# Kernel tuning notes

Measured on AMD Instinct MI355X. Metric: run time of the kernel, lower is better.

The kernel has to match this reference:

```python
import jax, jax.numpy as jnp
import numpy as np

BETA = 0.95
THRESH = 1.0
T = 25
MAXD = 11      # dilated_kernel_size: 250//25=10 -> bumped to odd 11
LP = 10        # left_pad = 250//25
B = 1024
SIGINIT = 5.0  # max_delay // 2, SIG is frozen at this value


@jax.custom_vjp
def atan_spike(u):
    # heaviside forward, atan surrogate gradient (snntorch surrogate.atan, alpha=2)
    return (u > 0).astype(u.dtype)

def _atan_fwd(u):
    return atan_spike(u), u

def _atan_bwd(u, g):
    return (g / (1.0 + (jnp.pi * u) ** 2),)

atan_spike.defvjp(_atan_fwd, _atan_bwd)


def dcls_kernel(W, P, SIG):
    # DCLS 'gauss': gaussian-interpolated dense kernel.
    # W: (O, I, kc), P/SIG: (1, O, I, kc) -> dense kernel (O, I, MAXD)
    idx = jnp.arange(MAXD, dtype=W.dtype)
    Pc = P[0] + MAXD // 2                      # center positions in dense kernel
    S = jnp.abs(SIG[0]) + 0.27                 # sigma floor (DCLS epsilon)
    X = jnp.exp(-0.5 * ((idx[:, None, None, None] - Pc) / S) ** 2)  # (K,O,I,kc)
    X = X / (X.sum(axis=0, keepdims=True) + 1e-7)
    return jnp.einsum('oic,joic->oij', W, X)


def dcls_conv(x, W, P, SIG, b):
    # x: (B, C_in, L) -> (B, C_out, L - MAXD + 1), VALID conv like padding=0
    k = dcls_kernel(W, P, SIG)
    y = jax.lax.conv_general_dilated(x, k, (1,), 'VALID',
                                     dimension_numbers=('NCH', 'OIH', 'NCH'))
    return y + b[None, :, None]


def batchnorm(x, gamma, beta, mean, var, eps=1e-5):
    # eval-mode BatchNorm1d over (B, C, L)
    inv = gamma / jnp.sqrt(var + eps)
    return (x - mean[None, :, None]) * inv[None, :, None] + beta[None, :, None]


def lif_scan(x):
    # snntorch Leaky, reset_mechanism='subtract'; x: (B, C, T) input currents
    xT = jnp.moveaxis(x, 2, 0)  # (T, B, C)

    def step(mem, xt):
        reset = jax.lax.stop_gradient(atan_spike(mem - THRESH))  # detached reset
        mem = BETA * mem + xt - reset * THRESH
        spk = atan_spike(mem - THRESH)
        return mem, (spk, mem)

    _, (spk, mem) = jax.lax.scan(step, jnp.zeros_like(xT[0]), xT)
    return spk, mem  # each (T, B, C)


def pad_left(x):
    return jnp.pad(x, ((0, 0), (0, 0), (LP, 0)))


def setup_inputs() -> dict:
    key = jax.random.key(0)
    ks = jax.random.split(key, 16)

    def w_init(k, o, i):
        return jax.random.normal(k, (o, i, 1), jnp.float32) / np.sqrt(i)

    inp = {
        'data': jax.random.normal(ks[0], (B, T, 140), jnp.float32),
        'W1': w_init(ks[1], 256, 140),
        'b1': jax.random.normal(ks[2], (256,), jnp.float32) * 0.01,
        'P1': jax.random.uniform(ks[3], (1, 256, 140, 1), jnp.float32, -SIGINIT, SIGINIT),
        'SIG1': jnp.full((1, 256, 140, 1), SIGINIT, jnp.float32),
        'bn1_gamma': jax.random.uniform(ks[4], (256,), jnp.float32, 0.5, 1.5),
        'bn1_beta': jax.random.normal(ks[5], (256,), jnp.float32) * 0.1,
        'bn1_mean': jax.random.normal(ks[6], (256,), jnp.float32) * 0.1,
        'bn1_var': jax.random.uniform(ks[7], (256,), jnp.float32, 0.5, 1.5),
        'W2': w_init(ks[8], 256, 256),
        'b2': jax.random.normal(ks[9], (256,), jnp.float32) * 0.01,
        'P2': jax.random.uniform(ks[10], (1, 256, 256, 1), jnp.float32, -SIGINIT, SIGINIT),
        'SIG2': jnp.full((1, 256, 256, 1), SIGINIT, jnp.float32),
        'bn2_gamma': jax.random.uniform(ks[11], (256,), jnp.float32, 0.5, 1.5),
        'bn2_beta': jax.random.normal(ks[12], (256,), jnp.float32) * 0.1,
        'bn2_mean': jax.random.normal(ks[13], (256,), jnp.float32) * 0.1,
        'bn2_var': jax.random.uniform(ks[14], (256,), jnp.float32, 0.5, 1.5),
        'W3': w_init(ks[15], 20, 256),
        'b3': jnp.zeros((20,), jnp.float32),
        'P3': jax.random.uniform(jax.random.fold_in(key, 99), (1, 20, 256, 1), jnp.float32, -SIGINIT, SIGINIT),
        'SIG3': jnp.full((1, 20, 256, 1), SIGINIT, jnp.float32),
    }
    return inp


def reference(data, W1, b1, P1, SIG1, bn1_gamma, bn1_beta, bn1_mean, bn1_var,
              W2, b2, P2, SIG2, bn2_gamma, bn2_beta, bn2_mean, bn2_var,
              W3, b3, P3, SIG3):
    # data: (B, T, 140); pad time dim on the left, then to (B, C, L)
    x = jnp.moveaxis(jnp.pad(data, ((0, 0), (LP, 0), (0, 0))), 1, 2)  # (B,140,T+LP)
    x = batchnorm(dcls_conv(x, W1, P1, SIG1, b1), bn1_gamma, bn1_beta, bn1_mean, bn1_var)
    spk1, _ = lif_scan(x)                  # (T, B, 256)
    in1 = jnp.moveaxis(spk1, 0, 2)         # (B, 256, T)  (dropout eval = identity)

    x = batchnorm(dcls_conv(pad_left(in1), W2, P2, SIG2, b2),
                  bn2_gamma, bn2_beta, bn2_mean, bn2_var)
    spk2, _ = lif_scan(x)
    in2 = jnp.moveaxis(spk2, 0, 2)         # (B, 256, T)

    x = dcls_conv(pad_left(in2), W3, P3, SIG3, b3)  # (B, 20, T)
    spk3, mem3 = lif_scan(x)               # (T, B, 20) each
    return spk3, mem3
```

## Files before the change

### kernel.cpp

```cpp
#include <hip/hip_runtime.h>
#include <math.h>

#define BB 1024
#define TT 25
#define LP 10
#define MAXD 11

#define XR2 26
#define XC 264
#define XSZ2 (XR2 * XC)

#define IC1 140
#define ICP1 160
#define XC1 168
#define XSZ1 (XR2 * XC1)
#define SS1 (2 * XSZ1)

typedef __bf16 bf16x8 __attribute__((ext_vector_type(8)));
typedef float  f32x4  __attribute__((ext_vector_type(4)));

#define MFMA16(A, B, C) __builtin_amdgcn_mfma_f32_16x16x32_bf16((A), (B), (C), 0, 0, 0)

__global__ void gen_trip(const float* __restrict__ W,
                         const float* __restrict__ P,
                         const float* __restrict__ SIG,
                         __bf16* __restrict__ Khi, __bf16* __restrict__ Kmid,
                         __bf16* __restrict__ Klo,
                         int O, int Opad, int I, int Ipad) {
    int idx = blockIdx.x * blockDim.x + threadIdx.x;
    if (idx >= Opad * Ipad) return;
    int i = idx % Ipad;
    int o = idx / Ipad;
    if (o >= O || i >= I) {
#pragma unroll
        for (int j = 0; j < MAXD; ++j) {
            size_t ofs = ((size_t)(j * Opad + o)) * Ipad + i;
            Khi[ofs] = (__bf16)0.0f;
            Kmid[ofs] = (__bf16)0.0f;
            Klo[ofs] = (__bf16)0.0f;
        }
        return;
    }
    int widx = o * I + i;
    float w  = W[widx];
    float pc = P[widx] + (float)(MAXD / 2);
    float s  = fabsf(SIG[widx]) + 0.27f;
    float x[MAXD];
    float sum = 0.f;
#pragma unroll
    for (int j = 0; j < MAXD; ++j) {
        float d = ((float)j - pc) / s;
        x[j] = expf(-0.5f * d * d);
        sum += x[j];
    }
    float denom = sum + 1e-7f;
#pragma unroll
    for (int j = 0; j < MAXD; ++j) {
        float kv = w * (x[j] / denom);
        __bf16 h = (__bf16)kv;
        float  r1 = kv - (float)h;
        __bf16 m = (__bf16)r1;
        float  r2 = r1 - (float)m;
        __bf16 l = (__bf16)r2;
        size_t ofs = ((size_t)(j * Opad + o)) * Ipad + i;
        Khi[ofs] = h;
        Kmid[ofs] = m;
        Klo[ofs] = l;
    }
}

__global__ __launch_bounds__(512, 2)
void conv1_mfma(const float* __restrict__ xin,
                const __bf16* __restrict__ Khi,
                const __bf16* __restrict__ Kmid,
                const __bf16* __restrict__ Klo,
                const float* __restrict__ bias,
                const float* __restrict__ gamma,
                const float* __restrict__ beta,
                const float* __restrict__ mean,
                const float* __restrict__ var,
                __bf16* __restrict__ spk1) {
    __shared__ __align__(16) char smem[3 * SS1 * 2];
    __bf16* xs = (__bf16*)smem;
    float*  ys = (float*)smem;

    const int b0   = blockIdx.x * 2;
    const int tid  = threadIdx.x;
    const int w    = tid >> 6;
    const int lane = tid & 63;
    const int lm   = lane & 15;
    const int quad = lane >> 4;

    {
        uint32_t* xz = (uint32_t*)smem;
        for (int k = tid; k < 3 * SS1 / 2; k += 512) xz[k] = 0u;
    }
    __syncthreads();
#pragma unroll
    for (int bl = 0; bl < 2; ++bl) {
        const float* src = xin + (size_t)(b0 + bl) * (TT * IC1);
        for (int k = tid; k < TT * IC1; k += 512) {
            int t = k / IC1;
            int i = k - t * IC1;
            float x  = src[k];
            __bf16 h = (__bf16)x;
            float r1 = x - (float)h;
            __bf16 m = (__bf16)r1;
            float r2 = r1 - (float)m;
            __bf16 l = (__bf16)r2;
            int ofs = bl * XSZ1 + t * XC1 + i;
            xs[0 * SS1 + ofs] = h;
            xs[1 * SS1 + ofs] = m;
            xs[2 * SS1 + ofs] = l;
        }
    }
    __syncthreads();

    f32x4 acc[2][4];
#pragma unroll
    for (int p = 0; p < 2; ++p)
#pragma unroll
        for (int nt = 0; nt < 4; ++nt) acc[p][nt] = (f32x4){0.f, 0.f, 0.f, 0.f};

    auto loadA = [&](int n, bf16x8* Ah, bf16x8* Am, bf16x8* Al) {
        n = (n > 54) ? 54 : n;
        const int j = n / 5;
        const int ic = n - 5 * j;
        const size_t base =
            (size_t)(j * 256 + w * 32 + lm) * ICP1 + ic * 32 + quad * 8;
#pragma unroll
        for (int p = 0; p < 2; ++p) {
            Ah[p] = *(const bf16x8*)(Khi  + base + p * 16 * ICP1);
            Am[p] = *(const bf16x8*)(Kmid + base + p * 16 * ICP1);
            Al[p] = *(const bf16x8*)(Klo  + base + p * 16 * ICP1);
        }
    };

    auto step = [&](int n, bf16x8* Ah, bf16x8* Am, bf16x8* Al) {
        const int j = n / 5;
        const int ic = n - 5 * j;
        int r0 = lm + j - 10;          r0 = ((unsigned)r0 < 25u) ? r0 : 25;
        int r1 = 16 + lm + j - 10;     r1 = ((unsigned)r1 < 25u) ? r1 : 25;
        const int col = ic * 32 + quad * 8;
#pragma unroll
        for (int bl = 0; bl < 2; ++bl) {
            bf16x8 Bh[2], Bm[2], Bl[2];
#pragma unroll
            for (int th = 0; th < 2; ++th) {
                const int row = th ? r1 : r0;
                const int ofs = bl * XSZ1 + row * XC1 + col;
                Bh[th] = *(const bf16x8*)&xs[0 * SS1 + ofs];
                Bm[th] = *(const bf16x8*)&xs[1 * SS1 + ofs];
                Bl[th] = *(const bf16x8*)&xs[2 * SS1 + ofs];
            }
#pragma unroll
            for (int p = 0; p < 2; ++p)
#pragma unroll
                for (int th = 0; th < 2; ++th)
                    acc[p][bl * 2 + th] = MFMA16(Ah[p], Bh[th], acc[p][bl * 2 + th]);
#pragma unroll
            for (int p = 0; p < 2; ++p)
#pragma unroll
                for (int th = 0; th < 2; ++th)
                    acc[p][bl * 2 + th] = MFMA16(Ah[p], Bm[th], acc[p][bl * 2 + th]);
#pragma unroll
            for (int p = 0; p < 2; ++p)
#pragma unroll
                for (int th = 0; th < 2; ++th)
                    acc[p][bl * 2 + th] = MFMA16(Am[p], Bh[th], acc[p][bl * 2 + th]);
#pragma unroll
            for (int p = 0; p < 2; ++p)
#pragma unroll
                for (int th = 0; th < 2; ++th)
                    acc[p][bl * 2 + th] = MFMA16(Ah[p], Bl[th], acc[p][bl * 2 + th]);
#pragma unroll
            for (int p = 0; p < 2; ++p)
#pragma unroll
                for (int th = 0; th < 2; ++th)
                    acc[p][bl * 2 + th] = MFMA16(Am[p], Bm[th], acc[p][bl * 2 + th]);
#pragma unroll
            for (int p = 0; p < 2; ++p)
#pragma unroll
                for (int th = 0; th < 2; ++th)
                    acc[p][bl * 2 + th] = MFMA16(Al[p], Bh[th], acc[p][bl * 2 + th]);
        }
    };

    bf16x8 A0h[2], A0m[2], A0l[2], A1h[2], A1m[2], A1l[2];
    loadA(0, A0h, A0m, A0l);
    for (int n = 0; n < 54; n += 2) {
        loadA(n + 1, A1h, A1m, A1l);
        step(n, A0h, A0m, A0l);
        loadA(n + 2, A0h, A0m, A0l);
        step(n + 1, A1h, A1m, A1l);
    }
    step(54, A0h, A0m, A0l);

#pragma unroll
    for (int bl = 0; bl < 2; ++bl) {
        __syncthreads();
#pragma unroll
        for (int p = 0; p < 2; ++p)
#pragma unroll
            for (int th = 0; th < 2; ++th) {
                int t = th * 16 + lm;
                if (t < TT) {
                    int ob = w * 32 + p * 16 + quad * 4;
#pragma unroll
                    for (int v = 0; v < 4; ++v)
                        ys[(ob + v) * 27 + t] = acc[p][bl * 2 + th][v];
                }
            }
        __syncthreads();
        if (tid < 256) {
            const int o = tid;
            float scale = gamma[o] / sqrtf(var[o] + 1e-5f);
            float ofs   = (bias[o] - mean[o]) * scale + beta[o];
            unsigned short* dst =
                (unsigned short*)spk1 + (size_t)(b0 + bl) * (TT * 256) + o;
            const float* yrow = &ys[o * 27];
            float memv = 0.f;
#pragma unroll
            for (int t = 0; t < TT; ++t) {
                float a     = yrow[t] * scale + ofs;
                float reset = (memv > 1.0f) ? 1.0f : 0.f;
                memv        = 0.95f * memv + a - reset;
                dst[t * 256] = (memv > 1.0f) ? 0x3F80 : 0;
            }
        }
    }
}

__global__ __launch_bounds__(512, 2)
void conv2_mfma(const __bf16* __restrict__ spk1,
                const __bf16* __restrict__ Khi,
                const __bf16* __restrict__ Kmid,
                const __bf16* __restrict__ Klo,
                const float* __restrict__ bias,
                const float* __restrict__ gamma,
                const float* __restrict__ beta,
                const float* __restrict__ mean,
                const float* __restrict__ var,
                __bf16* __restrict__ spk2) {
    __shared__ __align__(16) char smem[54912];
    __bf16* xs = (__bf16*)smem;
    float*  ys = (float*)smem;

    const int b0   = blockIdx.x * 4;
    const int tid  = threadIdx.x;
    const int w    = tid >> 6;
    const int lane = tid & 63;
    const int lm   = lane & 15;
    const int quad = lane >> 4;

    {
        uint32_t* xz = (uint32_t*)smem;
        for (int k = tid; k < 2 * XSZ2; k += 512) xz[k] = 0u;
    }
    __syncthreads();
#pragma unroll
    for (int bl = 0; bl < 4; ++bl) {
        const __bf16* src = spk1 + (size_t)(b0 + bl) * (TT * 256);
        for (int k = tid; k < TT * 256; k += 512) {
            int t = k >> 8, i = k & 255;
            xs[bl * XSZ2 + t * XC + i] = src[k];
        }
    }
    __syncthreads();

    f32x4 acc[2][8];
#pragma unroll
    for (int pi = 0; pi < 2; ++pi)
#pragma unroll
        for (int nt = 0; nt < 8; ++nt) acc[pi][nt] = (f32x4){0.f, 0.f, 0.f, 0.f};

    auto loadA = [&](int n, bf16x8* Ah, bf16x8* Am, bf16x8* Al) {
        n = (n > 87) ? 87 : n;
        const int j = n >> 3, ic = n & 7;
#pragma unroll
        for (int pi = 0; pi < 2; ++pi) {
            const size_t base =
                (size_t)(j * 256 + w * 32 + pi * 16 + lm) * 256 + ic * 32 + quad * 8;
            Ah[pi] = *(const bf16x8*)(Khi  + base);
            Am[pi] = *(const bf16x8*)(Kmid + base);
            Al[pi] = *(const bf16x8*)(Klo  + base);
        }
    };
    auto loadB = [&](int n, bf16x8* Bf) {
        const int j = n >> 3, ic = n & 7;
        int r0 = lm + j - 10;          r0 = ((unsigned)r0 < 25u) ? r0 : 25;
        int r1 = 16 + lm + j - 10;     r1 = ((unsigned)r1 < 25u) ? r1 : 25;
        const int col = ic * 32 + quad * 8;
#pragma unroll
        for (int bl = 0; bl < 4; ++bl) {
            Bf[bl * 2 + 0] = *(const bf16x8*)&xs[bl * XSZ2 + r0 * XC + col];
            Bf[bl * 2 + 1] = *(const bf16x8*)&xs[bl * XSZ2 + r1 * XC + col];
        }
    };
    auto compute = [&](bf16x8* Ah, bf16x8* Am, bf16x8* Al, bf16x8* Bf) {
#pragma unroll
        for (int pi = 0; pi < 2; ++pi)
#pragma unroll
            for (int nt = 0; nt < 8; ++nt)
                acc[pi][nt] = MFMA16(Ah[pi], Bf[nt], acc[pi][nt]);
#pragma unroll
        for (int pi = 0; pi < 2; ++pi)
#pragma unroll
            for (int nt = 0; nt < 8; ++nt)
                acc[pi][nt] = MFMA16(Am[pi], Bf[nt], acc[pi][nt]);
#pragma unroll
        for (int pi = 0; pi < 2; ++pi)
#pragma unroll
            for (int nt = 0; nt < 8; ++nt)
                acc[pi][nt] = MFMA16(Al[pi], Bf[nt], acc[pi][nt]);
    };

    bf16x8 A0h[2], A0m[2], A0l[2], A1h[2], A1m[2], A1l[2], B0[8], B1[8];
    loadA(0, A0h, A0m, A0l);
    loadB(0, B0);
    for (int n = 0; n < 86; n += 2) {
        loadA(n + 1, A1h, A1m, A1l);
        loadB(n + 1, B1);
        compute(A0h, A0m, A0l, B0);
        loadA(n + 2, A0h, A0m, A0l);
        loadB(n + 2, B0);
        compute(A1h, A1m, A1l, B1);
    }
    loadA(87, A1h, A1m, A1l);
    loadB(87, B1);
    compute(A0h, A0m, A0l, B0);
    compute(A1h, A1m, A1l, B1);

#pragma unroll
    for (int bl = 0; bl < 4; ++bl) {
        __syncthreads();
#pragma unroll
        for (int pi = 0; pi < 2; ++pi)
#pragma unroll
            for (int th = 0; th < 2; ++th) {
                int t = th * 16 + lm;
                if (t < TT) {
                    int ob = w * 32 + pi * 16 + quad * 4;
#pragma unroll
                    for (int v = 0; v < 4; ++v)
                        ys[(ob + v) * 27 + t] = acc[pi][bl * 2 + th][v];
                }
            }
        __syncthreads();
        if (tid < 256) {
            const int o = tid;
            float scale = gamma[o] / sqrtf(var[o] + 1e-5f);
            float ofs   = (bias[o] - mean[o]) * scale + beta[o];
            unsigned short* dst =
                (unsigned short*)spk2 + (size_t)(b0 + bl) * (TT * 256) + o;
            const float* yrow = &ys[o * 27];
            float memv = 0.f;
#pragma unroll
            for (int t = 0; t < TT; ++t) {
                float a     = yrow[t] * scale + ofs;
                float reset = (memv > 1.0f) ? 1.0f : 0.f;
                memv        = 0.95f * memv + a - reset;
                dst[t * 256] = (memv > 1.0f) ? 0x3F80 : 0;
            }
        }
    }
}

__global__ __launch_bounds__(512, 4)
void conv3_mfma(const __bf16* __restrict__ spk2,
                const __bf16* __restrict__ K3hi,
                const __bf16* __restrict__ K3mid,
                const __bf16* __restrict__ K3lo,
                const float* __restrict__ b3,
                float* __restrict__ out) {
    __shared__ __align__(16) __bf16 xs[2 * XSZ2];
    __shared__ float ys[2 * 32 * 27];

    const int b0   = blockIdx.x * 2;
    const int tid  = threadIdx.x;
    const int w    = tid >> 6;
    const int lane = tid & 63;
    const int lm   = lane & 15;
    const int quad = lane >> 4;

    {
        uint32_t* xz = (uint32_t*)xs;
        for (int k = tid; k < XSZ2; k += 512) xz[k] = 0u;
    }
    __syncthreads();
#pragma unroll
    for (int bl = 0; bl < 2; ++bl) {
        const __bf16* src = spk2 + (size_t)(b0 + bl) * (TT * 256);
        for (int k = tid; k < TT * 256; k += 512) {
            int t = k >> 8, i = k & 255;
            xs[bl * XSZ2 + t * XC + i] = src[k];
        }
    }
    __syncthreads();

    const int bl = w & 1;
    const int th = (w >> 1) & 1;
    const int p  = (w >> 2) & 1;

    f32x4 accH = (f32x4){0.f, 0.f, 0.f, 0.f};
    f32x4 accM = (f32x4){0.f, 0.f, 0.f, 0.f};
    f32x4 accL = (f32x4){0.f, 0.f, 0.f, 0.f};

    auto loadA = [&](int n, bf16x8* Ah, bf16x8* Am, bf16x8* Al) {
        n = (n > 87) ? 87 : n;
        const int j = n >> 3, ic = n & 7;
        const size_t kofs = ((size_t)(j * 32 + p * 16 + lm)) * 256 + ic * 32 + quad * 8;
        *Ah = *(const bf16x8*)(K3hi  + kofs);
        *Am = *(const bf16x8*)(K3mid + kofs);
        *Al = *(const bf16x8*)(K3lo  + kofs);
    };
    auto step = [&](int n, bf16x8 Ah, bf16x8 Am, bf16x8 Al) {
        const int j = n >> 3, ic = n & 7;
        int r = th * 16 + lm + j - 10;
        r = ((unsigned)r < 25u) ? r : 25;
        bf16x8 Bf = *(const bf16x8*)&xs[bl * XSZ2 + r * XC + ic * 32 + quad * 8];
        accH = MFMA16(Ah, Bf, accH);
        accM = MFMA16(Am, Bf, accM);
        accL = MFMA16(Al, Bf, accL);
    };

    bf16x8 A0h, A0m, A0l, A1h, A1m, A1l;
    loadA(0, &A0h, &A0m, &A0l);
    for (int n = 0; n < 86; n += 2) {
        loadA(n + 1, &A1h, &A1m, &A1l);
        step(n, A0h, A0m, A0l);
        loadA(n + 2, &A0h, &A0m, &A0l);
        step(n + 1, A1h, A1m, A1l);
    }
    loadA(87, &A1h, &A1m, &A1l);
    step(86, A0h, A0m, A0l);
    step(87, A1h, A1m, A1l);

    {
        int t = th * 16 + lm;
        if (t < TT) {
#pragma unroll
            for (int v = 0; v < 4; ++v)
                ys[(bl * 32 + p * 16 + quad * 4 + v) * 27 + t] =
                    accH[v] + accM[v] + accL[v];
        }
    }
    __syncthreads();

    if (tid < 40) {
        const int bl2 = tid / 20;
        const int o   = tid % 20;
        float memv = 0.f;
        float bo   = b3[o];
        const float* yrow = &ys[(bl2 * 32 + o) * 27];
#pragma unroll
        for (int t = 0; t < TT; ++t) {
            float a     = yrow[t] + bo;
            float reset = (memv > 1.0f) ? 1.0f : 0.f;
            memv        = 0.95f * memv + a - reset;
            float spk   = (memv > 1.0f) ? 1.0f : 0.f;
            out[(t * BB + (b0 + bl2)) * 20 + o]          = spk;
            out[TT * BB * 20 + (t * BB + (b0 + bl2)) * 20 + o] = memv;
        }
    }
}

extern "C" void kernel_launch(void* const* d_in, const int* in_sizes, int n_in,
                              void* d_out, int out_size, void* d_ws, size_t ws_size,
                              hipStream_t stream) {
    const float* data = (const float*)d_in[0];
    const float* W1   = (const float*)d_in[1];
    const float* b1   = (const float*)d_in[2];
    const float* P1   = (const float*)d_in[3];
    const float* SIG1 = (const float*)d_in[4];
    const float* g1   = (const float*)d_in[5];
    const float* be1  = (const float*)d_in[6];
    const float* m1   = (const float*)d_in[7];
    const float* v1   = (const float*)d_in[8];
    const float* W2   = (const float*)d_in[9];
    const float* b2   = (const float*)d_in[10];
    const float* P2   = (const float*)d_in[11];
    const float* SIG2 = (const float*)d_in[12];
    const float* g2   = (const float*)d_in[13];
    const float* be2  = (const float*)d_in[14];
    const float* m2   = (const float*)d_in[15];
    const float* v2   = (const float*)d_in[16];
    const float* W3   = (const float*)d_in[17];
    const float* b3   = (const float*)d_in[18];
    const float* P3   = (const float*)d_in[19];
    const float* SIG3 = (const float*)d_in[20];
    float* out = (float*)d_out;

    char* p = (char*)d_ws;
    __bf16* K1hi  = (__bf16*)p;  p += 901120;
    __bf16* K1mid = (__bf16*)p;  p += 901120;
    __bf16* K1lo  = (__bf16*)p;  p += 901120;
    __bf16* spk1  = (__bf16*)p;  p += 13107200;
    __bf16* spk2  = (__bf16*)p;  p += 13107200;
    __bf16* K2hi  = (__bf16*)p;  p += 1441792;
    __bf16* K2mid = (__bf16*)p;  p += 1441792;
    __bf16* K2lo  = (__bf16*)p;  p += 1441792;
    __bf16* K3hi  = (__bf16*)p;  p += 180224;
    __bf16* K3mid = (__bf16*)p;  p += 180224;
    __bf16* K3lo  = (__bf16*)p;

    gen_trip<<<(256 * 160 + 255) / 256, 256, 0, stream>>>(
        W1, P1, SIG1, K1hi, K1mid, K1lo, 256, 256, 140, 160);
    gen_trip<<<(256 * 256 + 255) / 256, 256, 0, stream>>>(
        W2, P2, SIG2, K2hi, K2mid, K2lo, 256, 256, 256, 256);
    gen_trip<<<(32 * 256 + 255) / 256, 256, 0, stream>>>(
        W3, P3, SIG3, K3hi, K3mid, K3lo, 20, 32, 256, 256);

    conv1_mfma<<<BB / 2, 512, 0, stream>>>(data, K1hi, K1mid, K1lo,
                                           b1, g1, be1, m1, v1, spk1);
    conv2_mfma<<<BB / 4, 512, 0, stream>>>(spk1, K2hi, K2mid, K2lo,
                                           b2, g2, be2, m2, v2, spk2);
    conv3_mfma<<<BB / 2, 512, 0, stream>>>(spk2, K3hi, K3mid, K3lo, b3, out);
}
```

Baseline: 498.7 us.

## Fuse conv2 and conv3 into one kernel keeping spikes in shared memory

```diff
diff --git a/kernel.cpp b/kernel.cpp
--- a/kernel.cpp
+++ b/kernel.cpp
@@ -232,19 +232,24 @@
 }
 
 __global__ __launch_bounds__(512, 2)
-void conv2_mfma(const __bf16* __restrict__ spk1,
-                const __bf16* __restrict__ Khi,
-                const __bf16* __restrict__ Kmid,
-                const __bf16* __restrict__ Klo,
-                const float* __restrict__ bias,
-                const float* __restrict__ gamma,
-                const float* __restrict__ beta,
-                const float* __restrict__ mean,
-                const float* __restrict__ var,
-                __bf16* __restrict__ spk2) {
-    __shared__ __align__(16) char smem[54912];
-    __bf16* xs = (__bf16*)smem;
-    float*  ys = (float*)smem;
+void conv23_mfma(const __bf16* __restrict__ spk1,
+                 const __bf16* __restrict__ Khi,
+                 const __bf16* __restrict__ Kmid,
+                 const __bf16* __restrict__ Klo,
+                 const float* __restrict__ bias,
+                 const float* __restrict__ gamma,
+                 const float* __restrict__ beta,
+                 const float* __restrict__ mean,
+                 const float* __restrict__ var,
+                 const __bf16* __restrict__ K3hi,
+                 const __bf16* __restrict__ K3mid,
+                 const __bf16* __restrict__ K3lo,
+                 const float* __restrict__ b3,
+                 float* __restrict__ out) {
+    __shared__ __align__(16) char smem[61568];
+    __bf16* xs  = (__bf16*)smem;
+    float*  ysq = (float*)(smem + 54912);
+    float*  ys3 = (float*)smem;
 
     const int b0   = blockIdx.x * 4;
     const int tid  = threadIdx.x;
@@ -253,214 +258,199 @@
     const int lm   = lane & 15;
     const int quad = lane >> 4;
 
+    for (int k = tid; k < 4 * (XC / 2); k += 512) {
+        int bl = k / (XC / 2);
+        int c  = k % (XC / 2);
+        ((uint32_t*)xs)[(bl * XSZ2 + 25 * XC) / 2 + c] = 0u;
+    }
+    for (int k = tid; k < 4 * 800; k += 512) {
+        int bl = k / 800;
+        int v  = k % 800;
+        int t  = v >> 5;
+        int iv = v & 31;
+        uint4 d = ((const uint4*)(spk1 + (size_t)(b0 + bl) * (TT * 256)))[v];
+        *(uint4*)&xs[bl * XSZ2 + t * XC + iv * 8] = d;
+    }
+    __syncthreads();
+
+    f32x4 acc[2][8];
+#pragma unroll
+    for (int pi = 0; pi < 2; ++pi)
+#pragma unroll
+        for (int nt = 0; nt < 8; ++nt) acc[pi][nt] = (f32x4){0.f, 0.f, 0.f, 0.f};
+
     {
-        uint32_t* xz = (uint32_t*)smem;
-        for (int k = tid; k < 2 * XSZ2; k += 512) xz[k] = 0u;
+        auto loadA = [&](int n, bf16x8* Ah, bf16x8* Am, bf16x8* Al) {
+            n = (n > 87) ? 87 : n;
+            const int j = n >> 3, ic = n & 7;
+#pragma unroll
+            for (int pi = 0; pi < 2; ++pi) {
+                const size_t base =
+                    (size_t)(j * 256 + w * 32 + pi * 16 + lm) * 256 + ic * 32 + quad * 8;
+                Ah[pi] = *(const bf16x8*)(Khi  + base);
+                Am[pi] = *(const bf16x8*)(Kmid + base);
+                Al[pi] = *(const bf16x8*)(Klo  + base);
+            }
+        };
+        auto loadB = [&](int n, bf16x8* Bf) {
+            const int j = n >> 3, ic = n & 7;
+            int r0 = lm + j - 10;          r0 = ((unsigned)r0 < 25u) ? r0 : 25;
+            int r1 = 16 + lm + j - 10;     r1 = ((unsigned)r1 < 25u) ? r1 : 25;
+            const int col = ic * 32 + quad * 8;
+#pragma unroll
+            for (int bl = 0; bl < 4; ++bl) {
+                Bf[bl * 2 + 0] = *(const bf16x8*)&xs[bl * XSZ2 + r0 * XC + col];
+                Bf[bl * 2 + 1] = *(const bf16x8*)&xs[bl * XSZ2 + r1 * XC + col];
+            }
+        };
+        auto compute = [&](bf16x8* Ah, bf16x8* Am, bf16x8* Al, bf16x8* Bf) {
+#pragma unroll
+            for (int pi = 0; pi < 2; ++pi)
+#pragma unroll
+                for (int nt = 0; nt < 8; ++nt)
+                    acc[pi][nt] = MFMA16(Ah[pi], Bf[nt], acc[pi][nt]);
+#pragma unroll
+            for (int pi = 0; pi < 2; ++pi)
+#pragma unroll
+                for (int nt = 0; nt < 8; ++nt)
+                    acc[pi][nt] = MFMA16(Am[pi], Bf[nt], acc[pi][nt]);
+#pragma unroll
+            for (int pi = 0; pi < 2; ++pi)
+#pragma unroll
+                for (int nt = 0; nt < 8; ++nt)
+                    acc[pi][nt] = MFMA16(Al[pi], Bf[nt], acc[pi][nt]);
+        };
+
+        bf16x8 A0h[2], A0m[2], A0l[2], A1h[2], A1m[2], A1l[2], B0[8], B1[8];
+        loadA(0, A0h, A0m, A0l);
+        loadB(0, B0);
+        for (int n = 0; n < 86; n += 2) {
+            loadA(n + 1, A1h, A1m, A1l);
+            loadB(n + 1, B1);
+            compute(A0h, A0m, A0l, B0);
+            loadA(n + 2, A0h, A0m, A0l);
+            loadB(n + 2, B0);
+            compute(A1h, A1m, A1l, B1);
+        }
+        loadA(87, A1h, A1m, A1l);
+        loadB(87, B1);
+        compute(A0h, A0m, A0l, B0);
+        compute(A1h, A1m, A1l, B1);
+    }
+
+#pragma unroll
+    for (int bl = 0; bl < 4; ++bl) {
+#pragma unroll
+        for (int q = 0; q < 4; ++q) {
+            __syncthreads();
+            if ((w >> 1) == q) {
+#pragma unroll
+                for (int pi = 0; pi < 2; ++pi)
+#pragma unroll
+                    for (int th = 0; th < 2; ++th) {
+                        int t = th * 16 + lm;
+                        if (t < TT) {
+                            int ol = (w & 1) * 32 + pi * 16 + quad * 4;
+#pragma unroll
+                            for (int v = 0; v < 4; ++v)
+                                ysq[(ol + v) * 26 + t] = acc[pi][bl * 2 + th][v];
+                        }
+                    }
+            }
+            __syncthreads();
+            if (tid < 64) {
+                const int o = q * 64 + tid;
+                float scale = gamma[o] / sqrtf(var[o] + 1e-5f);
+                float ofs   = (bias[o] - mean[o]) * scale + beta[o];
+                const float* yrow = &ysq[tid * 26];
+                unsigned short* sx = (unsigned short*)xs;
+                float memv = 0.f;
+#pragma unroll
+                for (int t = 0; t < TT; ++t) {
+                    float a     = yrow[t] * scale + ofs;
+                    float reset = (memv > 1.0f) ? 1.0f : 0.f;
+                    memv        = 0.95f * memv + a - reset;
+                    sx[bl * XSZ2 + t * XC + o] = (memv > 1.0f) ? 0x3F80 : 0;
+                }
+            }
+        }
     }
     __syncthreads();
-#pragma unroll
-    for (int bl = 0; bl < 4; ++bl) {
-        const __bf16* src = spk1 + (size_t)(b0 + bl) * (TT * 256);
-        for (int k = tid; k < TT * 256; k += 512) {
-            int t = k >> 8, i = k & 255;
-            xs[bl * XSZ2 + t * XC + i] = src[k];
-        }
-    }
-    __syncthreads();
-
-    f32x4 acc[2][8];
-#pragma unroll
-    for (int pi = 0; pi < 2; ++pi)
-#pragma unroll
-        for (int nt = 0; nt < 8; ++nt) acc[pi][nt] = (f32x4){0.f, 0.f, 0.f, 0.f};
-
-    auto loadA = [&](int n, bf16x8* Ah, bf16x8* Am, bf16x8* Al) {
-        n = (n > 87) ? 87 : n;
-        const int j = n >> 3, ic = n & 7;
-#pragma unroll
-        for (int pi = 0; pi < 2; ++pi) {
-            const size_t base =
-                (size_t)(j * 256 + w * 32 + pi * 16 + lm) * 256 + ic * 32 + quad * 8;
-            Ah[pi] = *(const bf16x8*)(Khi  + base);
-            Am[pi] = *(const bf16x8*)(Kmid + base);
-            Al[pi] = *(const bf16x8*)(Klo  + base);
-        }
-    };
-    auto loadB = [&](int n, bf16x8* Bf) {
-        const int j = n >> 3, ic = n & 7;
-        int r0 = lm + j - 10;          r0 = ((unsigned)r0 < 25u) ? r0 : 25;
-        int r1 = 16 + lm + j - 10;     r1 = ((unsigned)r1 < 25u) ? r1 : 25;
-        const int col = ic * 32 + quad * 8;
-#pragma unroll
-        for (int bl = 0; bl < 4; ++bl) {
-            Bf[bl * 2 + 0] = *(const bf16x8*)&xs[bl * XSZ2 + r0 * XC + col];
-            Bf[bl * 2 + 1] = *(const bf16x8*)&xs[bl * XSZ2 + r1 * XC + col];
-        }
-    };
-    auto compute = [&](bf16x8* Ah, bf16x8* Am, bf16x8* Al, bf16x8* Bf) {
-#pragma unroll
-        for (int pi = 0; pi < 2; ++pi)
-#pragma unroll
-            for (int nt = 0; nt < 8; ++nt)
-                acc[pi][nt] = MFMA16(Ah[pi], Bf[nt], acc[pi][nt]);
-#pragma unroll
-        for (int pi = 0; pi < 2; ++pi)
-#pragma unroll
-            for (int nt = 0; nt < 8; ++nt)
-                acc[pi][nt] = MFMA16(Am[pi], Bf[nt], acc[pi][nt]);
-#pragma unroll
-        for (int pi = 0; pi < 2; ++pi)
-#pragma unroll
-            for (int nt = 0; nt < 8; ++nt)
-                acc[pi][nt] = MFMA16(Al[pi], Bf[nt], acc[pi][nt]);
-    };
-
-    bf16x8 A0h[2], A0m[2], A0l[2], A1h[2], A1m[2], A1l[2], B0[8], B1[8];
-    loadA(0, A0h, A0m, A0l);
-    loadB(0, B0);
-    for (int n = 0; n < 86; n += 2) {
-        loadA(n + 1, A1h, A1m, A1l);
-        loadB(n + 1, B1);
-        compute(A0h, A0m, A0l, B0);
-        loadA(n + 2, A0h, A0m, A0l);
-        loadB(n + 2, B0);
-        compute(A1h, A1m, A1l, B1);
-    }
-    loadA(87, A1h, A1m, A1l);
-    loadB(87, B1);
-    compute(A0h, A0m, A0l, B0);
-    compute(A1h, A1m, A1l, B1);
-
-#pragma unroll
-    for (int bl = 0; bl < 4; ++bl) {
+
+    {
+        const int p3  = w >> 2;
+        const int bl3 = w & 3;
+        f32x4 accH[2], accM[2], accL[2];
+#pragma unroll
+        for (int th = 0; th < 2; ++th) {
+            accH[th] = (f32x4){0.f, 0.f, 0.f, 0.f};
+            accM[th] = (f32x4){0.f, 0.f, 0.f, 0.f};
+            accL[th] = (f32x4){0.f, 0.f, 0.f, 0.f};
+        }
+
+        auto loadA3 = [&](int n, bf16x8* Ah, bf16x8* Am, bf16x8* Al) {
+            n = (n > 87) ? 87 : n;
+            const int j = n >> 3, ic = n & 7;
+            const size_t kofs =
+                ((size_t)(j * 32 + p3 * 16 + lm)) * 256 + ic * 32 + quad * 8;
+            *Ah = *(const bf16x8*)(K3hi  + kofs);
+            *Am = *(const bf16x8*)(K3mid + kofs);
+            *Al = *(const bf16x8*)(K3lo  + kofs);
+        };
+        auto step3 = [&](int n, bf16x8 Ah, bf16x8 Am, bf16x8 Al) {
+            const int j = n >> 3, ic = n & 7;
+#pragma unroll
+            for (int th = 0; th < 2; ++th) {
+                int r = th * 16 + lm + j - 10;
+                r = ((unsigned)r < 25u) ? r : 25;
+                bf16x8 Bf =
+                    *(const bf16x8*)&xs[bl3 * XSZ2 + r * XC + ic * 32 + quad * 8];
+                accH[th] = MFMA16(Ah, Bf, accH[th]);
+                accM[th] = MFMA16(Am, Bf, accM[th]);
+                accL[th] = MFMA16(Al, Bf, accL[th]);
+            }
+        };
+
+        bf16x8 A0h, A0m, A0l, A1h, A1m, A1l;
+        loadA3(0, &A0h, &A0m, &A0l);
+        for (int n = 0; n < 86; n += 2) {
+            loadA3(n + 1, &A1h, &A1m, &A1l);
+            step3(n, A0h, A0m, A0l);
+            loadA3(n + 2, &A0h, &A0m, &A0l);
+            step3(n + 1, A1h, A1m, A1l);
+        }
+        loadA3(87, &A1h, &A1m, &A1l);
+        step3(86, A0h, A0m, A0l);
+        step3(87, A1h, A1m, A1l);
+
         __syncthreads();
 #pragma unroll
-        for (int pi = 0; pi < 2; ++pi)
-#pragma unroll
-            for (int th = 0; th < 2; ++th) {
-                int t = th * 16 + lm;
-                if (t < TT) {
-                    int ob = w * 32 + pi * 16 + quad * 4;
-#pragma unroll
-                    for (int v = 0; v < 4; ++v)
-                        ys[(ob + v) * 27 + t] = acc[pi][bl * 2 + th][v];
-                }
-            }
+        for (int th = 0; th < 2; ++th) {
+            int t = th * 16 + lm;
+            if (t < TT) {
+#pragma unroll
+                for (int v = 0; v < 4; ++v)
+                    ys3[(bl3 * 32 + p3 * 16 + quad * 4 + v) * 26 + t] =
+                        accH[th][v] + accM[th][v] + accL[th][v];
+            }
+        }
         __syncthreads();
-        if (tid < 256) {
-            const int o = tid;
-            float scale = gamma[o] / sqrtf(var[o] + 1e-5f);
-            float ofs   = (bias[o] - mean[o]) * scale + beta[o];
-            unsigned short* dst =
-                (unsigned short*)spk2 + (size_t)(b0 + bl) * (TT * 256) + o;
-            const float* yrow = &ys[o * 27];
+
+        if (tid < 80) {
+            const int bl2 = tid / 20;
+            const int o   = tid % 20;
             float memv = 0.f;
+            float bo   = b3[o];
+            const float* yrow = &ys3[(bl2 * 32 + o) * 26];
 #pragma unroll
             for (int t = 0; t < TT; ++t) {
-                float a     = yrow[t] * scale + ofs;
+                float a     = yrow[t] + bo;
                 float reset = (memv > 1.0f) ? 1.0f : 0.f;
                 memv        = 0.95f * memv + a - reset;
-                dst[t * 256] = (memv > 1.0f) ? 0x3F80 : 0;
-            }
-        }
-    }
-}
-
-__global__ __launch_bounds__(512, 4)
-void conv3_mfma(const __bf16* __restrict__ spk2,
-                const __bf16* __restrict__ K3hi,
-                const __bf16* __restrict__ K3mid,
-                const __bf16* __restrict__ K3lo,
-                const float* __restrict__ b3,
-                float* __restrict__ out) {
-    __shared__ __align__(16) __bf16 xs[2 * XSZ2];
-    __shared__ float ys[2 * 32 * 27];
-
-    const int b0   = blockIdx.x * 2;
-    const int tid  = threadIdx.x;
-    const int w    = tid >> 6;
-    const int lane = tid & 63;
-    const int lm   = lane & 15;
-    const int quad = lane >> 4;
-
-    {
-        uint32_t* xz = (uint32_t*)xs;
-        for (int k = tid; k < XSZ2; k += 512) xz[k] = 0u;
-    }
-    __syncthreads();
-#pragma unroll
-    for (int bl = 0; bl < 2; ++bl) {
-        const __bf16* src = spk2 + (size_t)(b0 + bl) * (TT * 256);
-        for (int k = tid; k < TT * 256; k += 512) {
-            int t = k >> 8, i = k & 255;
-            xs[bl * XSZ2 + t * XC + i] = src[k];
-        }
-    }
-    __syncthreads();
-
-    const int bl = w & 1;
-    const int th = (w >> 1) & 1;
-    const int p  = (w >> 2) & 1;
-
-    f32x4 accH = (f32x4){0.f, 0.f, 0.f, 0.f};
-    f32x4 accM = (f32x4){0.f, 0.f, 0.f, 0.f};
-    f32x4 accL = (f32x4){0.f, 0.f, 0.f, 0.f};
-
-    auto loadA = [&](int n, bf16x8* Ah, bf16x8* Am, bf16x8* Al) {
-        n = (n > 87) ? 87 : n;
-        const int j = n >> 3, ic = n & 7;
-        const size_t kofs = ((size_t)(j * 32 + p * 16 + lm)) * 256 + ic * 32 + quad * 8;
-        *Ah = *(const bf16x8*)(K3hi  + kofs);
-        *Am = *(const bf16x8*)(K3mid + kofs);
-        *Al = *(const bf16x8*)(K3lo  + kofs);
-    };
-    auto step = [&](int n, bf16x8 Ah, bf16x8 Am, bf16x8 Al) {
-        const int j = n >> 3, ic = n & 7;
-        int r = th * 16 + lm + j - 10;
-        r = ((unsigned)r < 25u) ? r : 25;
-        bf16x8 Bf = *(const bf16x8*)&xs[bl * XSZ2 + r * XC + ic * 32 + quad * 8];
-        accH = MFMA16(Ah, Bf, accH);
-        accM = MFMA16(Am, Bf, accM);
-        accL = MFMA16(Al, Bf, accL);
-    };
-
-    bf16x8 A0h, A0m, A0l, A1h, A1m, A1l;
-    loadA(0, &A0h, &A0m, &A0l);
-    for (int n = 0; n < 86; n += 2) {
-        loadA(n + 1, &A1h, &A1m, &A1l);
-        step(n, A0h, A0m, A0l);
-        loadA(n + 2, &A0h, &A0m, &A0l);
-        step(n + 1, A1h, A1m, A1l);
-    }
-    loadA(87, &A1h, &A1m, &A1l);
-    step(86, A0h, A0m, A0l);
-    step(87, A1h, A1m, A1l);
-
-    {
-        int t = th * 16 + lm;
-        if (t < TT) {
-#pragma unroll
-            for (int v = 0; v < 4; ++v)
-                ys[(bl * 32 + p * 16 + quad * 4 + v) * 27 + t] =
-                    accH[v] + accM[v] + accL[v];
-        }
-    }
-    __syncthreads();
-
-    if (tid < 40) {
-        const int bl2 = tid / 20;
-        const int o   = tid % 20;
-        float memv = 0.f;
-        float bo   = b3[o];
-        const float* yrow = &ys[(bl2 * 32 + o) * 27];
-#pragma unroll
-        for (int t = 0; t < TT; ++t) {
-            float a     = yrow[t] + bo;
-            float reset = (memv > 1.0f) ? 1.0f : 0.f;
-            memv        = 0.95f * memv + a - reset;
-            float spk   = (memv > 1.0f) ? 1.0f : 0.f;
-            out[(t * BB + (b0 + bl2)) * 20 + o]          = spk;
-            out[TT * BB * 20 + (t * BB + (b0 + bl2)) * 20 + o] = memv;
+                float spk   = (memv > 1.0f) ? 1.0f : 0.f;
+                out[(t * BB + (b0 + bl2)) * 20 + o]               = spk;
+                out[TT * BB * 20 + (t * BB + (b0 + bl2)) * 20 + o] = memv;
+            }
         }
     }
 }
@@ -496,7 +486,6 @@
     __bf16* K1mid = (__bf16*)p;  p += 901120;
     __bf16* K1lo  = (__bf16*)p;  p += 901120;
     __bf16* spk1  = (__bf16*)p;  p += 13107200;
-    __bf16* spk2  = (__bf16*)p;  p += 13107200;
     __bf16* K2hi  = (__bf16*)p;  p += 1441792;
     __bf16* K2mid = (__bf16*)p;  p += 1441792;
     __bf16* K2lo  = (__bf16*)p;  p += 1441792;
@@ -513,7 +502,7 @@
 
     conv1_mfma<<<BB / 2, 512, 0, stream>>>(data, K1hi, K1mid, K1lo,
                                            b1, g1, be1, m1, v1, spk1);
-    conv2_mfma<<<BB / 4, 512, 0, stream>>>(spk1, K2hi, K2mid, K2lo,
-                                           b2, g2, be2, m2, v2, spk2);
-    conv3_mfma<<<BB / 2, 512, 0, stream>>>(spk2, K3hi, K3mid, K3lo, b3, out);
+    conv23_mfma<<<BB / 4, 512, 0, stream>>>(spk1, K2hi, K2mid, K2lo,
+                                            b2, g2, be2, m2, v2,
+                                            K3hi, K3mid, K3lo, b3, out);
 }
```

After: 435.6 us. 1.14x faster.
